# Kernel tuning notes

Hardware: AMD Instinct MI355X
Metric: run time of the kernel (lower is better)

## Reference

```python
import jax, jax.numpy as jnp
import numpy as np

LEAKY_SLOPE = 0.01  # torch F.leaky_relu default
LN_EPS = 1e-5       # torch nn.LayerNorm default


def _layer_norm(x, g, b):
    mu = jnp.mean(x, axis=-1, keepdims=True)
    var = jnp.var(x, axis=-1, keepdims=True)
    return (x - mu) * jax.lax.rsqrt(var + LN_EPS) * g + b


def _gcn(x, adj, W, b):
    # GraphConvolution (Kipf-style): adj @ (x @ W) + b
    return adj @ (x @ W) + b


def setup_inputs() -> dict:
    key = jax.random.key(0)
    ks = jax.random.split(key, 8)
    N, fan_in, fan_mid, fan_out = 12288, 128, 128, 20
    h0, h1, h2 = fan_mid, fan_mid // 2, fan_mid // 4  # 128, 64, 32
    inp = {
        "x": jax.random.normal(ks[0], (N, fan_in), dtype=jnp.float32),
        "adj0": jax.random.uniform(ks[1], (N, N), dtype=jnp.float32),
        "adj1": jax.random.uniform(ks[2], (N, N), dtype=jnp.float32),
        "adj2": jax.random.uniform(ks[3], (N, N), dtype=jnp.float32),
        "W0": jax.random.normal(ks[4], (fan_in, h0), dtype=jnp.float32) / np.sqrt(fan_in),
        "b0": jnp.zeros((h0,), dtype=jnp.float32),
        "W1": jax.random.normal(ks[5], (h0, h1), dtype=jnp.float32) / np.sqrt(h0),
        "b1": jnp.zeros((h1,), dtype=jnp.float32),
        "W2": jax.random.normal(ks[6], (h1, h2), dtype=jnp.float32) / np.sqrt(h1),
        "b2": jnp.zeros((h2,), dtype=jnp.float32),
        "g0": jnp.ones((h0,), dtype=jnp.float32),
        "be0": jnp.zeros((h0,), dtype=jnp.float32),
        "g1": jnp.ones((h1,), dtype=jnp.float32),
        "be1": jnp.zeros((h1,), dtype=jnp.float32),
        "g2": jnp.ones((h2,), dtype=jnp.float32),
        "be2": jnp.zeros((h2,), dtype=jnp.float32),
        "Wl": jax.random.normal(ks[7], (h2, fan_out), dtype=jnp.float32) / np.sqrt(h2),
        "bl": jnp.zeros((fan_out,), dtype=jnp.float32),
    }
    return inp


def reference(x, adj0, adj1, adj2, W0, b0, W1, b1, W2, b2,
              g0, be0, g1, be1, g2, be2, Wl, bl):
    # first GCN + LayerNorm (no activation, matching the original forward)
    h = _layer_norm(_gcn(x, adj0, W0, b0), g0, be0)
    # two loop iterations: GCN -> LN -> LeakyReLU -> Dropout(eval=identity)
    h = jax.nn.leaky_relu(_layer_norm(_gcn(h, adj1, W1, b1), g1, be1), LEAKY_SLOPE)
    h = jax.nn.leaky_relu(_layer_norm(_gcn(h, adj2, W2, b2), g2, be2), LEAKY_SLOPE)
    logits = h @ Wl + bl
    return jax.nn.log_softmax(logits, axis=1)
```

## Files before the change

### kernel.cpp

```cpp
#include <hip/hip_runtime.h>
#include <cstdint>
#include <cstddef>

typedef __attribute__((ext_vector_type(8))) short short8;
typedef __attribute__((ext_vector_type(4))) float f32x4;

#define DEV __device__ __forceinline__

DEV unsigned short f2bf(float f) {
  unsigned int u = __float_as_uint(f);
  u += 0x7fffu + ((u >> 16) & 1u);
  return (unsigned short)(u >> 16);
}

DEV void glds16(const void* g, void* l) {
  __builtin_amdgcn_global_load_lds(
      (const __attribute__((address_space(1))) void*)g,
      (__attribute__((address_space(3))) void*)l, 16, 0, 0);
}

constexpr int NROW = 12288;

__global__ __launch_bounds__(256) void xw_kernel(
    const float* __restrict__ x, const float* __restrict__ W0,
    unsigned short* __restrict__ t0T) {
  __shared__ float sW[128 * 128];
  __shared__ float sx[16][128];
  const int t = threadIdx.x;
  for (int i = t; i < 128 * 128; i += 256) sW[i] = W0[i];
  const int r0 = blockIdx.x * 16;
  for (int i = t; i < 16 * 128; i += 256)
    sx[i >> 7][i & 127] = x[(size_t)(r0 + (i >> 7)) * 128 + (i & 127)];
  __syncthreads();
  const int c = t & 127;
  const int rg = t >> 7;
  float acc[8] = {0, 0, 0, 0, 0, 0, 0, 0};
  for (int k = 0; k < 128; ++k) {
    float w = sW[k * 128 + c];
#pragma unroll
    for (int j = 0; j < 8; ++j) acc[j] += sx[rg * 8 + j][k] * w;
  }
  uint4 o;
  unsigned int p[4];
#pragma unroll
  for (int q = 0; q < 4; ++q)
    p[q] = (unsigned int)f2bf(acc[2 * q]) |
           ((unsigned int)f2bf(acc[2 * q + 1]) << 16);
  o.x = p[0]; o.y = p[1]; o.z = p[2]; o.w = p[3];
  *(uint4*)(t0T + (size_t)c * NROW + r0 + rg * 8) = o;
}

template <int H>
__global__ __launch_bounds__(256, 3) void gcn_gemm(
    const float* __restrict__ A, const unsigned short* __restrict__ BT,
    float* __restrict__ part) {
  constexpr int KSPLIT = 4;
  constexpr int BM = 64, BK = 64;
  constexpr int WN = (H >= 64) ? 2 : 1;
  constexpr int WM = 4 / WN;
  constexpr int MR = BM / (WM * 16);
  constexpr int NR = H / (WN * 16);
  constexpr int NB = H / 32;
  constexpr int KSTEPS = (NROW / KSPLIT) / BK;
  constexpr int BBYTES = H * 128;

  __shared__ alignas(16) char lds[16384 + 2 * BBYTES];
  char* ldsB = lds + 16384;

  const int t = threadIdx.x;
  const int nmb = NROW / BM;
  const int bm = blockIdx.x % nmb;
  const int split = blockIdx.x / nmb;
  const int k0 = split * (NROW / KSPLIT);

  const int mA = t >> 4;
  const int kA = (t & 15) * 4;
  const float* aptr = A + (size_t)(bm * BM + mA) * NROW + k0 + kA;
  int aw[4];
#pragma unroll
  for (int i = 0; i < 4; ++i) {
    int row = i * 16 + mA;
    aw[i] = ((row * 128) + kA * 2) ^ ((row & 7) << 4);
  }

  const int nB0 = t >> 3;
  const int wB = (t & 7) ^ (nB0 & 7);
  const unsigned short* bptr = BT + (size_t)nB0 * NROW + k0 + wB * 8;
  const int wid = t >> 6;
  char* ldsBw = ldsB + wid * 1024;

  const int lane = t & 63;
  const int l15 = lane & 15;
  const int loct = lane >> 4;
  const int wm = wid / WN;
  const int wn = wid % WN;
  int aoff[MR][2], boff[NR][2];
#pragma unroll
  for (int m = 0; m < MR; ++m)
#pragma unroll
    for (int kk = 0; kk < 2; ++kk) {
      int row = wm * (MR * 16) + m * 16 + l15;
      aoff[m][kk] = (row * 128 + kk * 64 + loct * 16) ^ ((row & 7) << 4);
    }
#pragma unroll
  for (int n = 0; n < NR; ++n)
#pragma unroll
    for (int kk = 0; kk < 2; ++kk) {
      int nn = wn * (NR * 16) + n * 16 + l15;
      boff[n][kk] = (nn * 128 + kk * 64 + loct * 16) ^ ((nn & 7) << 4);
    }

  f32x4 acc[MR][NR];
#pragma unroll
  for (int m = 0; m < MR; ++m)
#pragma unroll
    for (int n = 0; n < NR; ++n) acc[m][n] = {0.f, 0.f, 0.f, 0.f};

  float4 av0[4], av1[4];

  auto gloadA = [&](float4* av, int s) {
#pragma unroll
    for (int i = 0; i < 4; ++i)
      av[i] = *(const float4*)(aptr + (size_t)i * 16 * NROW + s * BK);
  };
  auto glB = [&](int s, int buf) {
#pragma unroll
    for (int j = 0; j < NB; ++j)
      glds16(bptr + (size_t)j * 32 * NROW + s * BK,
             ldsBw + buf * BBYTES + j * 4096);
  };
  auto lstoreA = [&](const float4* av, int buf) {
    char* lA = lds + buf * 8192;
#pragma unroll
    for (int i = 0; i < 4; ++i) {
      uint2 w;
      w.x = (unsigned int)f2bf(av[i].x) | ((unsigned int)f2bf(av[i].y) << 16);
      w.y = (unsigned int)f2bf(av[i].z) | ((unsigned int)f2bf(av[i].w) << 16);
      *(uint2*)(lA + aw[i]) = w;
    }
  };
  auto compute = [&](int buf) {
    const char* lA = lds + buf * 8192;
    const char* lB = ldsB + buf * BBYTES;
#pragma unroll
    for (int kk = 0; kk < 2; ++kk) {
      short8 af[MR], bfv[NR];
#pragma unroll
      for (int m = 0; m < MR; ++m) af[m] = *(const short8*)(lA + aoff[m][kk]);
#pragma unroll
      for (int n = 0; n < NR; ++n) bfv[n] = *(const short8*)(lB + boff[n][kk]);
#pragma unroll
      for (int m = 0; m < MR; ++m)
#pragma unroll
        for (int n = 0; n < NR; ++n)
          acc[m][n] = __builtin_amdgcn_mfma_f32_16x16x32_bf16(
              af[m], bfv[n], acc[m][n], 0, 0, 0);
    }
  };

  glB(0, 0);
  gloadA(av0, 0);
  lstoreA(av0, 0);
  gloadA(av1, 1);
  asm volatile("s_waitcnt lgkmcnt(0)" ::: "memory");
  __builtin_amdgcn_s_barrier();
  __builtin_amdgcn_sched_barrier(0);

  static_assert((KSTEPS & 1) == 0, "KSTEPS must be even");
  for (int s = 0; s + 2 < KSTEPS; s += 2) {
    glB(s + 1, 1);
    gloadA(av0, s + 2);
    compute(0);
    lstoreA(av1, 1);
    asm volatile("s_waitcnt vmcnt(4) lgkmcnt(0)" ::: "memory");
    __builtin_amdgcn_s_barrier();
    __builtin_amdgcn_sched_barrier(0);
    glB(s + 2, 0);
    gloadA(av1, s + 3);
    compute(1);
    lstoreA(av0, 0);
    asm volatile("s_waitcnt vmcnt(4) lgkmcnt(0)" ::: "memory");
    __builtin_amdgcn_s_barrier();
    __builtin_amdgcn_sched_barrier(0);
  }

  glB(KSTEPS - 1, 1);
  compute(0);
  lstoreA(av1, 1);
  asm volatile("s_waitcnt vmcnt(0) lgkmcnt(0)" ::: "memory");
  __builtin_amdgcn_s_barrier();
  __builtin_amdgcn_sched_barrier(0);
  compute(1);

  float* pout = part + ((size_t)split * NROW + (size_t)bm * BM) * H;
#pragma unroll
  for (int m = 0; m < MR; ++m) {
    const int row = wm * (MR * 16) + m * 16 + loct * 4;
#pragma unroll
    for (int n = 0; n < NR; ++n) {
      const int col = wn * (NR * 16) + n * 16 + l15;
#pragma unroll
      for (int r = 0; r < 4; ++r)
        pout[(size_t)(row + r) * H + col] = acc[m][n][r];
    }
  }
}

template <int H, int H2, bool ACT>
__global__ __launch_bounds__(256) void reduce_ln(
    const float* __restrict__ part, const float* __restrict__ bias,
    const float* __restrict__ g, const float* __restrict__ be,
    const float* __restrict__ Wn, unsigned short* __restrict__ tT) {
  __shared__ float sW[H * H2];
  __shared__ float sh[4][H];
  const int t = threadIdx.x;
  for (int i = t; i < H * H2; i += 256) sW[i] = Wn[i];
  __syncthreads();

  const int wid = t >> 6, lane = t & 63;
  const int row = blockIdx.x * 4 + wid;
  constexpr int CPL = H / 64;
  float v[CPL];
#pragma unroll
  for (int c = 0; c < CPL; ++c) {
    const int col = lane + c * 64;
    float s = bias[col];
#pragma unroll
    for (int sp = 0; sp < 4; ++sp)
      s += part[((size_t)sp * NROW + row) * H + col];
    v[c] = s;
  }
  float sum = 0;
#pragma unroll
  for (int c = 0; c < CPL; ++c) sum += v[c];
#pragma unroll
  for (int o = 32; o > 0; o >>= 1) sum += __shfl_xor(sum, o);
  const float mu = sum / H;
  float vs = 0;
#pragma unroll
  for (int c = 0; c < CPL; ++c) { float d = v[c] - mu; vs += d * d; }
#pragma unroll
  for (int o = 32; o > 0; o >>= 1) vs += __shfl_xor(vs, o);
  const float rstd = rsqrtf(vs / H + 1e-5f);
#pragma unroll
  for (int c = 0; c < CPL; ++c) {
    const int col = lane + c * 64;
    float h = (v[c] - mu) * rstd * g[col] + be[col];
    if (ACT) h = (h > 0.f) ? h : 0.01f * h;
    sh[wid][col] = h;
  }
  __syncthreads();
  if (lane < H2) {
    float d = 0;
#pragma unroll 8
    for (int k = 0; k < H; ++k) d += sh[wid][k] * sW[k * H2 + lane];
    tT[(size_t)lane * NROW + row] = f2bf(d);
  }
}

__global__ __launch_bounds__(256) void reduce_final(
    const float* __restrict__ part, const float* __restrict__ bias,
    const float* __restrict__ g, const float* __restrict__ be,
    const float* __restrict__ Wl, const float* __restrict__ bl,
    float* __restrict__ out) {
  __shared__ float sW[32 * 20];
  __shared__ float sbl[20];
  __shared__ float sh[4][32];
  __shared__ float sl[4][20];
  const int t = threadIdx.x;
  for (int i = t; i < 640; i += 256) sW[i] = Wl[i];
  if (t < 20) sbl[t] = bl[t];
  __syncthreads();
  const int wid = t >> 6, lane = t & 63;
  const int row = blockIdx.x * 4 + wid;
  const int col = lane & 31;
  float v = bias[col];
#pragma unroll
  for (int sp = 0; sp < 4; ++sp)
    v += part[((size_t)sp * NROW + row) * 32 + col];
  float sum = v;
#pragma unroll
  for (int o = 32; o > 0; o >>= 1) sum += __shfl_xor(sum, o);
  const float mu = sum / 64.f;
  float d0 = v - mu;
  float vs = d0 * d0;
#pragma unroll
  for (int o = 32; o > 0; o >>= 1) vs += __shfl_xor(vs, o);
  const float rstd = rsqrtf(vs / 64.f + 1e-5f);
  float h = (v - mu) * rstd * g[col] + be[col];
  h = (h > 0.f) ? h : 0.01f * h;
  if (lane < 32) sh[wid][col] = h;
  __syncthreads();
  if (lane < 20) {
    float lg = sbl[lane];
#pragma unroll
    for (int k = 0; k < 32; ++k) lg += sh[wid][k] * sW[k * 20 + lane];
    sl[wid][lane] = lg;
  }
  __syncthreads();
  if (lane < 20) {
    float mx = -1e30f;
#pragma unroll
    for (int k = 0; k < 20; ++k) mx = fmaxf(mx, sl[wid][k]);
    float se = 0.f;
#pragma unroll
    for (int k = 0; k < 20; ++k) se += expf(sl[wid][k] - mx);
    out[(size_t)row * 20 + lane] = sl[wid][lane] - mx - logf(se);
  }
}

extern "C" void kernel_launch(void* const* d_in, const int* in_sizes, int n_in,
                              void* d_out, int out_size, void* d_ws,
                              size_t ws_size, hipStream_t stream) {
  const float* x    = (const float*)d_in[0];
  const float* adj0 = (const float*)d_in[1];
  const float* adj1 = (const float*)d_in[2];
  const float* adj2 = (const float*)d_in[3];
  const float* W0   = (const float*)d_in[4];
  const float* b0   = (const float*)d_in[5];
  const float* W1   = (const float*)d_in[6];
  const float* b1   = (const float*)d_in[7];
  const float* W2   = (const float*)d_in[8];
  const float* b2   = (const float*)d_in[9];
  const float* g0   = (const float*)d_in[10];
  const float* be0  = (const float*)d_in[11];
  const float* g1   = (const float*)d_in[12];
  const float* be1  = (const float*)d_in[13];
  const float* g2   = (const float*)d_in[14];
  const float* be2  = (const float*)d_in[15];
  const float* Wl   = (const float*)d_in[16];
  const float* bl   = (const float*)d_in[17];
  float* out = (float*)d_out;

  char* ws = (char*)d_ws;
  float* part =          (float*)(ws);
  unsigned short* t0T = (unsigned short*)(ws + 25165824);
  unsigned short* t1T = (unsigned short*)(ws + 25165824 + 3145728);
  unsigned short* t2T = (unsigned short*)(ws + 25165824 + 3145728 + 1572864);

  xw_kernel<<<NROW / 16, 256, 0, stream>>>(x, W0, t0T);
  gcn_gemm<128><<<(NROW / 64) * 4, 256, 0, stream>>>(adj0, t0T, part);
  reduce_ln<128, 64, false><<<NROW / 4, 256, 0, stream>>>(part, b0, g0, be0, W1, t1T);
  gcn_gemm<64><<<(NROW / 64) * 4, 256, 0, stream>>>(adj1, t1T, part);
  reduce_ln<64, 32, true><<<NROW / 4, 256, 0, stream>>>(part, b1, g1, be1, W2, t2T);
  gcn_gemm<32><<<(NROW / 64) * 4, 256, 0, stream>>>(adj2, t2T, part);
  reduce_final<<<NROW / 4, 256, 0, stream>>>(part, b2, g2, be2, Wl, bl, out);
}
```

Before: 483.5 us.

## Load A in contiguous 768-byte row chunks spanning three k-steps per super-step

Each thread now owns one A row and loads 12 float4 covering three BK=64 k-steps (768 contiguous bytes) at once, instead of four strided rows per k-step. The pipeline is restructured around super-steps of three k-steps, with bf16 conversion and 16-byte LDS writes per step. The intent is more contiguous, larger-granularity streaming of the fp32 adjacency matrix, which dominates memory traffic, and fewer issue points. In exchange, register pressure rises (12 float4) and several barriers now wait on vmcnt(0), which can stall the B prefetch and reduce overlap.

New measurement: 465.5 us. 1.04x faster.

```diff
diff --git a/kernel.cpp b/kernel.cpp
--- a/kernel.cpp
+++ b/kernel.cpp
@@ -11,6 +11,10 @@
   unsigned int u = __float_as_uint(f);
   u += 0x7fffu + ((u >> 16) & 1u);
   return (unsigned short)(u >> 16);
+}
+
+DEV unsigned int pk2(float a, float b) {
+  return (unsigned int)f2bf(a) | ((unsigned int)f2bf(b) << 16);
 }
 
 DEV void glds16(const void* g, void* l) {
@@ -41,12 +45,10 @@
     for (int j = 0; j < 8; ++j) acc[j] += sx[rg * 8 + j][k] * w;
   }
   uint4 o;
-  unsigned int p[4];
-#pragma unroll
-  for (int q = 0; q < 4; ++q)
-    p[q] = (unsigned int)f2bf(acc[2 * q]) |
-           ((unsigned int)f2bf(acc[2 * q + 1]) << 16);
-  o.x = p[0]; o.y = p[1]; o.z = p[2]; o.w = p[3];
+  o.x = pk2(acc[0], acc[1]);
+  o.y = pk2(acc[2], acc[3]);
+  o.z = pk2(acc[4], acc[5]);
+  o.w = pk2(acc[6], acc[7]);
   *(uint4*)(t0T + (size_t)c * NROW + r0 + rg * 8) = o;
 }
 
@@ -62,7 +64,9 @@
   constexpr int NR = H / (WN * 16);
   constexpr int NB = H / 32;
   constexpr int KSTEPS = (NROW / KSPLIT) / BK;
+  constexpr int NSUP = KSTEPS / 3;
   constexpr int BBYTES = H * 128;
+  static_assert(KSTEPS % 3 == 0, "");
 
   __shared__ alignas(16) char lds[16384 + 2 * BBYTES];
   char* ldsB = lds + 16384;
@@ -73,15 +77,11 @@
   const int split = blockIdx.x / nmb;
   const int k0 = split * (NROW / KSPLIT);
 
-  const int mA = t >> 4;
-  const int kA = (t & 15) * 4;
-  const float* aptr = A + (size_t)(bm * BM + mA) * NROW + k0 + kA;
-  int aw[4];
-#pragma unroll
-  for (int i = 0; i < 4; ++i) {
-    int row = i * 16 + mA;
-    aw[i] = ((row * 128) + kA * 2) ^ ((row & 7) << 4);
-  }
+  const int r = t >> 2, q = t & 3;
+  const float* aptr = A + (size_t)(bm * BM + r) * NROW + k0 + q * 16;
+  const int sw = (r & 7) << 4;
+  const int aw0 = (r * 128 + q * 32) ^ sw;
+  const int aw1 = (r * 128 + q * 32 + 16) ^ sw;
 
   const int nB0 = t >> 3;
   const int wB = (t & 7) ^ (nB0 & 7);
@@ -116,12 +116,14 @@
 #pragma unroll
     for (int n = 0; n < NR; ++n) acc[m][n] = {0.f, 0.f, 0.f, 0.f};
 
-  float4 av0[4], av1[4];
-
-  auto gloadA = [&](float4* av, int s) {
-#pragma unroll
-    for (int i = 0; i < 4; ++i)
-      av[i] = *(const float4*)(aptr + (size_t)i * 16 * NROW + s * BK);
+  float4 av[12];
+
+  auto issueSuper = [&](int S) {
+#pragma unroll
+    for (int j = 0; j < 3; ++j)
+#pragma unroll
+      for (int i = 0; i < 4; ++i)
+        av[j * 4 + i] = *(const float4*)(aptr + S * 192 + j * 64 + i * 4);
   };
   auto glB = [&](int s, int buf) {
 #pragma unroll
@@ -129,15 +131,19 @@
       glds16(bptr + (size_t)j * 32 * NROW + s * BK,
              ldsBw + buf * BBYTES + j * 4096);
   };
-  auto lstoreA = [&](const float4* av, int buf) {
-    char* lA = lds + buf * 8192;
-#pragma unroll
-    for (int i = 0; i < 4; ++i) {
-      uint2 w;
-      w.x = (unsigned int)f2bf(av[i].x) | ((unsigned int)f2bf(av[i].y) << 16);
-      w.y = (unsigned int)f2bf(av[i].z) | ((unsigned int)f2bf(av[i].w) << 16);
-      *(uint2*)(lA + aw[i]) = w;
-    }
+  auto cvtWrite = [&](int j, int buf) {
+    char* wb = lds + buf * 8192;
+    uint4 w0, w1;
+    w0.x = pk2(av[j * 4 + 0].x, av[j * 4 + 0].y);
+    w0.y = pk2(av[j * 4 + 0].z, av[j * 4 + 0].w);
+    w0.z = pk2(av[j * 4 + 1].x, av[j * 4 + 1].y);
+    w0.w = pk2(av[j * 4 + 1].z, av[j * 4 + 1].w);
+    w1.x = pk2(av[j * 4 + 2].x, av[j * 4 + 2].y);
+    w1.y = pk2(av[j * 4 + 2].z, av[j * 4 + 2].w);
+    w1.z = pk2(av[j * 4 + 3].x, av[j * 4 + 3].y);
+    w1.w = pk2(av[j * 4 + 3].z, av[j * 4 + 3].w);
+    *(uint4*)(wb + aw0) = w0;
+    *(uint4*)(wb + aw1) = w1;
   };
   auto compute = [&](int buf) {
     const char* lA = lds + buf * 8192;
@@ -158,39 +164,43 @@
     }
   };
 
+  issueSuper(0);
   glB(0, 0);
-  gloadA(av0, 0);
-  lstoreA(av0, 0);
-  gloadA(av1, 1);
-  asm volatile("s_waitcnt lgkmcnt(0)" ::: "memory");
-  __builtin_amdgcn_s_barrier();
-  __builtin_amdgcn_sched_barrier(0);
-
-  static_assert((KSTEPS & 1) == 0, "KSTEPS must be even");
-  for (int s = 0; s + 2 < KSTEPS; s += 2) {
-    glB(s + 1, 1);
-    gloadA(av0, s + 2);
-    compute(0);
-    lstoreA(av1, 1);
-    asm volatile("s_waitcnt vmcnt(4) lgkmcnt(0)" ::: "memory");
-    __builtin_amdgcn_s_barrier();
-    __builtin_amdgcn_sched_barrier(0);
-    glB(s + 2, 0);
-    gloadA(av1, s + 3);
-    compute(1);
-    lstoreA(av0, 0);
-    asm volatile("s_waitcnt vmcnt(4) lgkmcnt(0)" ::: "memory");
-    __builtin_amdgcn_s_barrier();
-    __builtin_amdgcn_sched_barrier(0);
-  }
-
-  glB(KSTEPS - 1, 1);
-  compute(0);
-  lstoreA(av1, 1);
+  cvtWrite(0, 0);
   asm volatile("s_waitcnt vmcnt(0) lgkmcnt(0)" ::: "memory");
   __builtin_amdgcn_s_barrier();
   __builtin_amdgcn_sched_barrier(0);
-  compute(1);
+
+  for (int S = 0; S < NSUP; ++S) {
+    const int b = S & 1;
+    glB(3 * S + 1, b ^ 1);
+    compute(b);
+    cvtWrite(1, b ^ 1);
+    asm volatile("s_waitcnt vmcnt(0) lgkmcnt(0)" ::: "memory");
+    __builtin_amdgcn_s_barrier();
+    __builtin_amdgcn_sched_barrier(0);
+    glB(3 * S + 2, b);
+    compute(b ^ 1);
+    cvtWrite(2, b);
+    if (S + 1 < NSUP) {
+      issueSuper(S + 1);
+      asm volatile("s_waitcnt vmcnt(12) lgkmcnt(0)" ::: "memory");
+    } else {
+      asm volatile("s_waitcnt vmcnt(0) lgkmcnt(0)" ::: "memory");
+    }
+    __builtin_amdgcn_s_barrier();
+    __builtin_amdgcn_sched_barrier(0);
+    if (S + 1 < NSUP) {
+      glB(3 * S + 3, b ^ 1);
+      compute(b);
+      cvtWrite(0, b ^ 1);
+      asm volatile("s_waitcnt vmcnt(0) lgkmcnt(0)" ::: "memory");
+      __builtin_amdgcn_s_barrier();
+      __builtin_amdgcn_sched_barrier(0);
+    } else {
+      compute(b);
+    }
+  }
 
   float* pout = part + ((size_t)split * NROW + (size_t)bm * BM) * H;
 #pragma unroll
@@ -200,8 +210,8 @@
     for (int n = 0; n < NR; ++n) {
       const int col = wn * (NR * 16) + n * 16 + l15;
 #pragma unroll
-      for (int r = 0; r < 4; ++r)
-        pout[(size_t)(row + r) * H + col] = acc[m][n][r];
+      for (int rr = 0; rr < 4; ++rr)
+        pout[(size_t)(row + rr) * H + col] = acc[m][n][rr];
     }
   }
 }
```
